# Kernel optimization log

Hardware: AMD Instinct MI355X
Metric: run time of the kernel (lower is better)

Reference implementation:

```python
import jax, jax.numpy as jnp
import numpy as np

C = 32          # d_model / channels
D_STATE = 32
D_CONV = 4
EXPAND = 2
D_INNER = EXPAND * C          # 64
DT_RANK = (C + 15) // 16      # ceil(32/16) = 2
EPS = 1e-5


def _conv2d(x, w, b):
    # x: (B,C,H,W), w: (O,I,3,3), stride 1, padding 1 (torch Conv2d)
    y = jax.lax.conv_general_dilated(
        x, w, window_strides=(1, 1), padding=[(1, 1), (1, 1)],
        dimension_numbers=("NCHW", "OIHW", "NCHW"))
    return y + b[None, :, None, None]


def _silu(x):
    return x * jax.nn.sigmoid(x)


def _mamba(xs, in_proj_w, conv1d_w, conv1d_b, x_proj_w, dt_proj_w, dt_proj_b,
           A_log, Dp, out_proj_w):
    # xs: (B, L, C)
    xz = xs @ in_proj_w.T                       # (B, L, 2*D_INNER)
    xm, z = jnp.split(xz, 2, axis=-1)           # each (B, L, D_INNER)

    # causal depthwise conv1d along L (torch: padding=d_conv-1 then [..., :L])
    xc = xm.transpose(0, 2, 1)                  # (B, D_INNER, L)
    xc = jax.lax.conv_general_dilated(
        xc, conv1d_w, window_strides=(1,), padding=[(D_CONV - 1, 0)],
        dimension_numbers=("NCH", "OIH", "NCH"),
        feature_group_count=D_INNER)
    xm = _silu((xc + conv1d_b[None, :, None]).transpose(0, 2, 1))  # (B,L,D_INNER)

    x_dbl = xm @ x_proj_w.T                     # (B, L, DT_RANK + 2*D_STATE)
    dt = x_dbl[..., :DT_RANK]
    Bm = x_dbl[..., DT_RANK:DT_RANK + D_STATE]  # (B, L, N)
    Cm = x_dbl[..., DT_RANK + D_STATE:]         # (B, L, N)

    delta = jax.nn.softplus(dt @ dt_proj_w.T + dt_proj_b)  # (B, L, D_INNER)
    A = -jnp.exp(A_log)                                     # (D_INNER, N)

    deltaA = jnp.exp(delta[..., None] * A)                           # (B,L,D,N)
    deltaBx = delta[..., None] * Bm[:, :, None, :] * xm[..., None]   # (B,L,D,N)

    def combine(c1, c2):
        a1, b1 = c1
        a2, b2 = c2
        return a1 * a2, a2 * b1 + b2

    # parallel linear recurrence h_t = deltaA_t * h_{t-1} + deltaBx_t
    _, hstate = jax.lax.associative_scan(combine, (deltaA, deltaBx), axis=1)

    y = jnp.einsum("bldn,bln->bld", hstate, Cm) + xm * Dp
    y = y * _silu(z)
    return y @ out_proj_w.T                     # (B, L, C)


def setup_inputs() -> dict:
    key = jax.random.key(0)
    ks = jax.random.split(key, 16)
    s = 0.02
    inp = {
        "x": jax.random.normal(ks[0], (4, C, 64, 64), dtype=jnp.float32),
        "conv1_w": jax.random.normal(ks[1], (2 * C, C, 3, 3), jnp.float32) * s,
        "conv1_b": jnp.zeros((2 * C,), jnp.float32),
        "conv2_w": jax.random.normal(ks[2], (C, 2 * C, 3, 3), jnp.float32) * s,
        "conv2_b": jnp.zeros((C,), jnp.float32),
        "ln_g": jnp.ones((C,), jnp.float32),
        "ln_b": jnp.zeros((C,), jnp.float32),
        "in_proj_w": jax.random.normal(ks[3], (2 * D_INNER, C), jnp.float32) * s,
        "conv1d_w": jax.random.normal(ks[4], (D_INNER, 1, D_CONV), jnp.float32) * 0.1,
        "conv1d_b": jnp.zeros((D_INNER,), jnp.float32),
        "x_proj_w": jax.random.normal(ks[5], (DT_RANK + 2 * D_STATE, D_INNER), jnp.float32) * s,
        "dt_proj_w": jax.random.normal(ks[6], (D_INNER, DT_RANK), jnp.float32) * 0.1,
        "dt_proj_b": jax.random.normal(ks[7], (D_INNER,), jnp.float32) * 0.1 - 4.0,
        "A_log": jnp.log(jnp.tile(jnp.arange(1, D_STATE + 1, dtype=jnp.float32), (D_INNER, 1))),
        "Dp": jnp.ones((D_INNER,), jnp.float32),
        "out_proj_w": jax.random.normal(ks[8], (C, D_INNER), jnp.float32) * s,
        "smooth_w": jax.random.normal(ks[9], (C, C, 3, 3), jnp.float32) * s,
        "smooth_b": jnp.zeros((C,), jnp.float32),
    }
    return inp


def reference(x, conv1_w, conv1_b, conv2_w, conv2_b, ln_g, ln_b,
              in_proj_w, conv1d_w, conv1d_b, x_proj_w, dt_proj_w, dt_proj_b,
              A_log, Dp, out_proj_w, smooth_w, smooth_b):
    b, c, h, w = x.shape
    # convb residual
    t = jax.nn.relu(_conv2d(x, conv1_w, conv1_b))
    x = _conv2d(t, conv2_w, conv2_b) + x
    # reshape (b,c,h,w) -> (b, h*w, c) row-major (faithful to torch .reshape)
    xs = x.reshape(b, -1, c)
    # LayerNorm over last dim
    mu = jnp.mean(xs, axis=-1, keepdims=True)
    var = jnp.mean(jnp.square(xs - mu), axis=-1, keepdims=True)
    xs = (xs - mu) * jax.lax.rsqrt(var + EPS) * ln_g + ln_b
    # Mamba block
    y = _mamba(xs, in_proj_w, conv1d_w, conv1d_b, x_proj_w, dt_proj_w,
               dt_proj_b, A_log, Dp, out_proj_w)
    y = y.transpose(0, 2, 1).reshape(b, c, h, w)
    return _conv2d(y, smooth_w, smooth_b)
```

## Files before the change

kernel.cpp:

```cpp
#include <hip/hip_runtime.h>
#include <math.h>

#define SEQL 4096
#define L2E 1.44269504088896340736f

#if defined(__has_builtin)
#if __has_builtin(__builtin_amdgcn_exp2f)
#define FAST_EXP2(x) __builtin_amdgcn_exp2f(x)
#endif
#endif
#ifndef FAST_EXP2
#define FAST_EXP2(x) exp2f(x)
#endif

__device__ __forceinline__ float sigmoid_f(float x){ return 1.0f/(1.0f+expf(-x)); }

template<int CI, int CO, int COG, bool RELU, bool RES>
__global__ __launch_bounds__(256) void conv3x3_k(const float* __restrict__ in,
    const float* __restrict__ wgt, const float* __restrict__ bias,
    const float* __restrict__ res, float* __restrict__ out)
{
  constexpr int CIT = CI/4;
  __shared__ float tin[4][2][6][72];
  __shared__ float red[3][4][COG][66];
  const int tid  = threadIdx.x;
  const int lane = tid & 63;
  const int ty   = tid >> 6;
  const int tyu  = __builtin_amdgcn_readfirstlane(ty);
  const int h0   = blockIdx.x * 4;
  const int co0  = blockIdx.y * COG;
  const int b    = blockIdx.z;

  if (lane < 24){
    int cl = lane / 12, rem = lane % 12, r = rem >> 1, side = rem & 1;
    tin[ty][cl][r][side ? 68 : 3] = 0.0f;
  }

  float acc[4][COG];
  #pragma unroll
  for (int rr=0;rr<4;++rr)
    #pragma unroll
    for (int u=0;u<COG;++u) acc[rr][u] = 0.0f;

  const int ci0 = tyu*CIT;
  for (int cig = ci0; cig < ci0 + CIT; cig += 2){
    #pragma unroll
    for (int k=0;k<3;++k){
      int idx4 = lane + (k<<6);
      int row  = idx4 >> 4;
      int cl = row/6, r = row - cl*6;
      int w4 = (idx4 & 15) << 2;
      int h  = h0 - 1 + r;
      float4 v = make_float4(0.f,0.f,0.f,0.f);
      if (h>=0 && h<64)
        v = *(const float4*)(in + ((size_t)(b*CI+cig+cl)*64 + h)*64 + w4);
      *(float4*)&tin[ty][cl][r][4+w4] = v;
    }
    #pragma unroll
    for (int cl=0; cl<2; ++cl){
      float rv[6][3];
      #pragma unroll
      for (int r=0;r<6;++r)
        #pragma unroll
        for (int c=0;c<3;++c)
          rv[r][c] = tin[ty][cl][r][3+lane+c];
      #pragma unroll
      for (int u=0;u<COG;++u){
        const float* wp = wgt + ((size_t)(co0+u)*CI + cig + cl)*9;
        #pragma unroll
        for (int rr=0;rr<4;++rr)
          #pragma unroll
          for (int j=0;j<3;++j){
            acc[rr][u] = fmaf(rv[rr+j][0], wp[3*j+0], acc[rr][u]);
            acc[rr][u] = fmaf(rv[rr+j][1], wp[3*j+1], acc[rr][u]);
            acc[rr][u] = fmaf(rv[rr+j][2], wp[3*j+2], acc[rr][u]);
          }
      }
    }
  }
  if (ty > 0){
    #pragma unroll
    for (int rr=0;rr<4;++rr)
      #pragma unroll
      for (int u=0;u<COG;++u) red[ty-1][rr][u][lane] = acc[rr][u];
  }
  __syncthreads();
  if (ty == 0){
    #pragma unroll
    for (int rr=0;rr<4;++rr)
      #pragma unroll
      for (int u=0;u<COG;++u){
        float s = acc[rr][u] + red[0][rr][u][lane] + red[1][rr][u][lane]
                + red[2][rr][u][lane] + bias[co0+u];
        size_t ob = ((size_t)(b*CO+co0+u)*64 + h0+rr)*64 + lane;
        if constexpr (RES)  s += res[ob];
        if constexpr (RELU) s = fmaxf(s, 0.0f);
        out[ob] = s;
      }
  }
}

__global__ __launch_bounds__(1024, 4) void mamba_in_k(const float* __restrict__ x2,
    const float* __restrict__ g, const float* __restrict__ be,
    const float* __restrict__ Wip, const float* __restrict__ cw,
    const float* __restrict__ cb, const float* __restrict__ Wxp,
    const float* __restrict__ Wdt, const float* __restrict__ bdt,
    const float* __restrict__ A_log,
    float* __restrict__ xm2, float* __restrict__ szb, float* __restrict__ dlt,
    float* __restrict__ Bm, float* __restrict__ Cm,
    float* __restrict__ cA, float* __restrict__ cH)
{
  __shared__ __align__(16) float xn[68][37];
  __shared__ __align__(16) float xm[64][68];
  __shared__ __align__(16) float xtT[64][68];
  __shared__ __align__(16) float xd[64][67];
  float (*xbT)[68] = reinterpret_cast<float(*)[68]>(&xn[0][0]);
  const int tid = threadIdx.x, lane = tid & 63, ty = tid >> 6;
  const int tyu = __builtin_amdgcn_readfirstlane(ty);
  const int bi = blockIdx.x >> 6;
  const int l0 = (blockIdx.x & 63) << 6;

  {
    const int row = tid >> 3, sub = tid & 7;
    if (row < 67){
      const int tok = l0 - 3 + row;
      const int c0 = sub << 2;
      if (tok >= 0){
        float4 f = *(const float4*)(x2 + (size_t)bi*131072 + (size_t)tok*32 + c0);
        float s = (f.x+f.y)+(f.z+f.w);
        s += __shfl_xor(s,1); s += __shfl_xor(s,2); s += __shfl_xor(s,4);
        const float mu = s * 0.03125f;
        float dx=f.x-mu, dy=f.y-mu, dz=f.z-mu, dw=f.w-mu;
        float q = (dx*dx+dy*dy)+(dz*dz+dw*dw);
        q += __shfl_xor(q,1); q += __shfl_xor(q,2); q += __shfl_xor(q,4);
        const float rstd = 1.0f/sqrtf(q*0.03125f + 1e-5f);
        float4 gv = *(const float4*)(g  + c0);
        float4 bv = *(const float4*)(be + c0);
        xn[row][c0+0] = dx*rstd*gv.x + bv.x;
        xn[row][c0+1] = dy*rstd*gv.y + bv.y;
        xn[row][c0+2] = dz*rstd*gv.z + bv.z;
        xn[row][c0+3] = dw*rstd*gv.w + bv.w;
      } else {
        xn[row][c0+0]=0.0f; xn[row][c0+1]=0.0f;
        xn[row][c0+2]=0.0f; xn[row][c0+3]=0.0f;
      }
    }
  }
  __syncthreads();

  if (ty < 8){
    const int d0 = tyu*8;
    float xvA[32];
    #pragma unroll
    for (int c=0;c<32;++c) xvA[c] = xn[lane][c];
    #pragma unroll
    for (int jj=0;jj<8;++jj){
      const float4* wr = (const float4*)(Wip + (d0+jj)*32);
      float a = 0.0f;
      #pragma unroll
      for (int c4=0;c4<8;++c4){
        float4 w = wr[c4];
        a = fmaf(xvA[c4*4+0], w.x, a);
        a = fmaf(xvA[c4*4+1], w.y, a);
        a = fmaf(xvA[c4*4+2], w.z, a);
        a = fmaf(xvA[c4*4+3], w.w, a);
      }
      xm[d0+jj][lane] = a;
    }
    if (lane < 3){
      float xvB[32];
      #pragma unroll
      for (int c=0;c<32;++c) xvB[c] = xn[64+lane][c];
      #pragma unroll
      for (int jj=0;jj<8;++jj){
        const float4* wr = (const float4*)(Wip + (d0+jj)*32);
        float a = 0.0f;
        #pragma unroll
        for (int c4=0;c4<8;++c4){
          float4 w = wr[c4];
          a = fmaf(xvB[c4*4+0], w.x, a);
          a = fmaf(xvB[c4*4+1], w.y, a);
          a = fmaf(xvB[c4*4+2], w.z, a);
          a = fmaf(xvB[c4*4+3], w.w, a);
        }
        xm[d0+jj][64+lane] = a;
      }
    }
  } else {
    const int d0z = (tyu-8)*8;
    float xvC[32];
    #pragma unroll
    for (int c=0;c<32;++c) xvC[c] = xn[lane+3][c];
    #pragma unroll
    for (int jj=0;jj<8;++jj){
      const float4* wr = (const float4*)(Wip + (64+d0z+jj)*32);
      float a = 0.0f;
      #pragma unroll
      for (int c4=0;c4<8;++c4){
        float4 w = wr[c4];
        a = fmaf(xvC[c4*4+0], w.x, a);
        a = fmaf(xvC[c4*4+1], w.y, a);
        a = fmaf(xvC[c4*4+2], w.z, a);
        a = fmaf(xvC[c4*4+3], w.w, a);
      }
      szb[((size_t)(bi*64+d0z+jj))*SEQL + l0 + lane] = a * sigmoid_f(a);
    }
  }
  __syncthreads();

  #pragma unroll
  for (int jj=0;jj<4;++jj){
    int d = tyu*4 + jj;
    float4 w = *(const float4*)(cw + d*4);
    float a = xm[d][lane]*w.x + xm[d][lane+1]*w.y
            + xm[d][lane+2]*w.z + xm[d][lane+3]*w.w + cb[d];
    float s = a * sigmoid_f(a);
    xtT[d][lane] = s;
    xm2[((size_t)(bi*64+d))*SEQL + l0 + lane] = s;
  }
  __syncthreads();

  {
    float xv[64];
    #pragma unroll
    for (int c=0;c<64;++c) xv[c] = xtT[c][lane];
    for (int j=tyu; j<66; j+=16){
      const float4* wr = (const float4*)(Wxp + j*64);
      float a = 0.0f;
      #pragma unroll
      for (int c4=0;c4<16;++c4){
        float4 w = wr[c4];
        a = fmaf(xv[c4*4+0], w.x, a);
        a = fmaf(xv[c4*4+1], w.y, a);
        a = fmaf(xv[c4*4+2], w.z, a);
        a = fmaf(xv[c4*4+3], w.w, a);
      }
      xd[lane][j] = a;
    }
  }
  __syncthreads();

  {
    float dt0 = xd[lane][0], dt1 = xd[lane][1];
    #pragma unroll
    for (int k=0;k<4;++k){
      int d2 = tyu*4 + k;
      float2 wd = *(const float2*)(Wdt + d2*2);
      float v = dt0*wd.x + dt1*wd.y + bdt[d2];
      float sp = fmaxf(v,0.0f) + log1pf(expf(-fabsf(v)));
      dlt[((size_t)(bi*64+d2))*SEQL + l0 + lane] = sp;
      xm[d2][lane] = sp;
    }
    const int which = tyu >> 3, gq = tyu & 7;
    float* dst = which ? Cm : Bm;
    size_t base = ((size_t)bi*SEQL + l0 + lane)*32 + gq*4;
    const int s2 = 2 + which*32;
    float4 f0;
    f0.x = xd[lane][s2+gq+ 0]; f0.y = xd[lane][s2+gq+ 8];
    f0.z = xd[lane][s2+gq+16]; f0.w = xd[lane][s2+gq+24];
    *(float4*)(dst + base) = f0;
    if (!which){
      xbT[gq     ][lane] = f0.x;
      xbT[gq +  8][lane] = f0.y;
      xbT[gq + 16][lane] = f0.z;
      xbT[gq + 24][lane] = f0.w;
    }
  }
  __syncthreads();

  {
    const int d  = tid >> 4;
    const int gg = tid & 15;
    const int chunk = blockIdx.x & 63;
    const int bd = bi*64 + d;
    float Av0 = -expf(A_log[d*32 + gg     ]) * L2E;
    float Av1 = -expf(A_log[d*32 + gg + 16]) * L2E;
    float h0=0.0f, h1=0.0f, aP0=1.0f, aP1=1.0f;
    #pragma unroll 2
    for (int t0=0;t0<64;t0+=4){
      float4 dl4 = *(const float4*)&xm [d    ][t0];
      float4 xs4 = *(const float4*)&xtT[d    ][t0];
      float4 b04 = *(const float4*)&xbT[gg   ][t0];
      float4 b14 = *(const float4*)&xbT[gg+16][t0];
      #pragma unroll
      for (int k=0;k<4;++k){
        float dlv = (k==0)? dl4.x : (k==1)? dl4.y : (k==2)? dl4.z : dl4.w;
        float xsv = (k==0)? xs4.x : (k==1)? xs4.y : (k==2)? xs4.z : xs4.w;
        float bv0 = (k==0)? b04.x : (k==1)? b04.y : (k==2)? b04.z : b04.w;
        float bv1 = (k==0)? b14.x : (k==1)? b14.y : (k==2)? b14.z : b14.w;
        float m  = dlv * xsv;
        float a0 = FAST_EXP2(dlv*Av0);
        float a1 = FAST_EXP2(dlv*Av1);
        h0 = fmaf(a0, h0, m*bv0);  aP0 *= a0;
        h1 = fmaf(a1, h1, m*bv1);  aP1 *= a1;
      }
    }
    size_t base = ((size_t)bd*64 + chunk)*32;
    cA[base + gg] = aP0; cA[base + gg + 16] = aP1;
    cH[base + gg] = h0;  cH[base + gg + 16] = h1;
  }
}

__global__ __launch_bounds__(256) void scan_p2(const float* __restrict__ dlt,
    const float* __restrict__ xssm, const float* __restrict__ Bm,
    const float* __restrict__ Cm, const float* __restrict__ A_log,
    const float* __restrict__ Dp, const float* __restrict__ sz,
    const float* __restrict__ cA, const float* __restrict__ cHs,
    float* __restrict__ yt)
{
  __shared__ float pre[32][34];
  const int tid = threadIdx.x;
  const int grp = blockIdx.x & 1;
  const int bd  = blockIdx.x >> 1;
  const int b = bd >> 6, d = bd & 63;
  const int c0 = grp << 5;

  if (tid < 32){
    const float* pa = cA  + (size_t)bd*2048 + tid;
    const float* ph = cHs + (size_t)bd*2048 + tid;
    float hrun = 0.0f;
    if (grp){
      #pragma unroll 4
      for (int c=0;c<32;++c)
        hrun = fmaf(pa[c*32], hrun, ph[c*32]);
    }
    #pragma unroll 4
    for (int k=0;k<32;++k){
      pre[tid][k] = hrun;
      hrun = fmaf(pa[(c0+k)*32], hrun, ph[(c0+k)*32]);
    }
  }
  __syncthreads();

  const int lc = tid >> 3, gg = tid & 7;
  const int chunk = c0 + lc;
  const int l0 = chunk << 6;
  const float Dv = Dp[d];
  float Av2[4], h[4];
  #pragma unroll
  for (int j=0;j<4;++j){
    Av2[j] = -expf(A_log[d*32 + gg + 8*j]) * L2E;
    h[j] = pre[gg + 8*j][lc];
  }
  const float* del = dlt  + (size_t)bd*SEQL + l0;
  const float* xp  = xssm + (size_t)bd*SEQL + l0;
  const float* szp = sz   + (size_t)bd*SEQL + l0;
  const float* Bp  = Bm + ((size_t)b*SEQL + l0)*32 + gg*4;
  const float* Cp  = Cm + ((size_t)b*SEQL + l0)*32 + gg*4;
  float* yp = yt + (size_t)bd*SEQL + l0;

  for (int i0=0;i0<64;i0+=16){
    float4 y4[4];
    #pragma unroll
    for (int s=0;s<4;++s){
      const int ib = i0 + s*4;
      float4 d4 = *(const float4*)(del+ib);
      float4 x4 = *(const float4*)(xp +ib);
      float4 s4 = *(const float4*)(szp+ib);
      #pragma unroll
      for (int t=0;t<4;++t){
        float dl = (t==0)? d4.x : (t==1)? d4.y : (t==2)? d4.z : d4.w;
        float xl = (t==0)? x4.x : (t==1)? x4.y : (t==2)? x4.z : x4.w;
        float sl = (t==0)? s4.x : (t==1)? s4.y : (t==2)? s4.z : s4.w;
        float4 bv = *(const float4*)(Bp + (ib+t)*32);
        float4 cv = *(const float4*)(Cp + (ib+t)*32);
        float a0 = FAST_EXP2(dl*Av2[0]); h[0] = fmaf(a0, h[0], dl*bv.x*xl);
        float a1 = FAST_EXP2(dl*Av2[1]); h[1] = fmaf(a1, h[1], dl*bv.y*xl);
        float a2 = FAST_EXP2(dl*Av2[2]); h[2] = fmaf(a2, h[2], dl*bv.z*xl);
        float a3 = FAST_EXP2(dl*Av2[3]); h[3] = fmaf(a3, h[3], dl*bv.w*xl);
        float v = fmaf(h[3], cv.w, fmaf(h[2], cv.z, fmaf(h[1], cv.y, h[0]*cv.x)));
        v += __shfl_xor(v,1); v += __shfl_xor(v,2); v += __shfl_xor(v,4);
        float yv = fmaf(xl, Dv, v) * sl;
        if      (t==0) y4[s].x = yv;
        else if (t==1) y4[s].y = yv;
        else if (t==2) y4[s].z = yv;
        else           y4[s].w = yv;
      }
    }
    if (gg < 4){
      float4 w = (gg==0) ? y4[0] : (gg==1) ? y4[1] : (gg==2) ? y4[2] : y4[3];
      *(float4*)(yp + i0 + gg*4) = w;
    }
  }
}

__global__ __launch_bounds__(512) void outproj_k(const float* __restrict__ yt,
    const float* __restrict__ Wout, float* __restrict__ ym)
{
  __shared__ float ys[64][67];
  const int tid = threadIdx.x, lane = tid & 63, ty = tid >> 6;
  const int tyu = __builtin_amdgcn_readfirstlane(ty);
  const int bi = blockIdx.x >> 6;
  const int l0 = (blockIdx.x & 63) << 6;
  for (int r=ty; r<64; r+=8)
    ys[lane][r] = yt[((size_t)(bi*64+r))*SEQL + l0 + lane];
  __syncthreads();
  float yv[64];
  #pragma unroll
  for (int c=0;c<64;++c) yv[c] = ys[lane][c];
  #pragma unroll
  for (int jj=0;jj<4;++jj){
    int j = tyu*4 + jj;
    const float4* wr = (const float4*)(Wout + j*64);
    float acc = 0.0f;
    #pragma unroll
    for (int c4=0;c4<16;++c4){
      float4 w = wr[c4];
      acc = fmaf(yv[c4*4+0], w.x, acc);
      acc = fmaf(yv[c4*4+1], w.y, acc);
      acc = fmaf(yv[c4*4+2], w.z, acc);
      acc = fmaf(yv[c4*4+3], w.w, acc);
    }
    ym[((size_t)(bi*32+j))*SEQL + l0 + lane] = acc;
  }
}

extern "C" void kernel_launch(void* const* d_in, const int* in_sizes, int n_in,
                              void* d_out, int out_size, void* d_ws, size_t ws_size,
                              hipStream_t stream) {
  const float* x        = (const float*)d_in[0];
  const float* conv1_w  = (const float*)d_in[1];
  const float* conv1_b  = (const float*)d_in[2];
  const float* conv2_w  = (const float*)d_in[3];
  const float* conv2_b  = (const float*)d_in[4];
  const float* ln_g     = (const float*)d_in[5];
  const float* ln_b     = (const float*)d_in[6];
  const float* in_proj_w= (const float*)d_in[7];
  const float* conv1d_w = (const float*)d_in[8];
  const float* conv1d_b = (const float*)d_in[9];
  const float* x_proj_w = (const float*)d_in[10];
  const float* dt_proj_w= (const float*)d_in[11];
  const float* dt_proj_b= (const float*)d_in[12];
  const float* A_log    = (const float*)d_in[13];
  const float* Dp       = (const float*)d_in[14];
  const float* out_proj_w=(const float*)d_in[15];
  const float* smooth_w = (const float*)d_in[16];
  const float* smooth_b = (const float*)d_in[17];
  float* out = (float*)d_out;

  float* ws = (float*)d_ws;
  float* t      = ws;
  float* x2     = t      + 1048576;
  float* xm2    = x2     + 524288;
  float* szb    = xm2    + 1048576;
  float* dlt    = szb    + 1048576;
  float* Bmat   = dlt    + 1048576;
  float* Cmat   = Bmat   + 524288;
  float* yt     = Cmat   + 524288;
  float* ym     = yt     + 1048576;
  float* cA     = t;
  float* cH     = t + 524288;

  conv3x3_k<32,64,4,true ,false><<<dim3(16,16,4), 256, 0, stream>>>(x,  conv1_w, conv1_b, nullptr, t);
  conv3x3_k<64,32,4,false,true ><<<dim3(16,8,4), 256, 0, stream>>>(t,  conv2_w, conv2_b, x,       x2);
  mamba_in_k  <<<256, 1024, 0, stream>>>(x2, ln_g, ln_b, in_proj_w, conv1d_w, conv1d_b,
                                         x_proj_w, dt_proj_w, dt_proj_b, A_log,
                                         xm2, szb, dlt, Bmat, Cmat, cA, cH);
  scan_p2     <<<512, 256, 0, stream>>>(dlt, xm2, Bmat, Cmat, A_log, Dp, szb, cA, cH, yt);
  outproj_k   <<<256, 512, 0, stream>>>(yt, out_proj_w, ym);
  conv3x3_k<32,32,4,false,false><<<dim3(16,8,4), 256, 0, stream>>>(ym, smooth_w, smooth_b, nullptr, out);
}
```

Baseline: 192.1 us.

## Fuse chunked scan second pass with output projection in one kernel

Replaces the separate scan pass-2 and out-projection kernels with a single kernel. Each block handles one batch and one 64-token chunk for all 64 channels, stages delta, x, z, B and C through shared memory, computes each thread's chunk-prefix state by serially combining earlier chunk summaries, and applies the out projection directly from shared memory. This removes the intermediate y buffer round trip through global memory and one kernel launch. The cost is a per-thread serial prefix loop of up to 63 steps over chunk summaries, which adds redundant global reads and latency for later chunks.

```diff
diff --git a/kernel.cpp b/kernel.cpp
--- a/kernel.cpp
+++ b/kernel.cpp
@@ -301,117 +301,110 @@
   }
 }
 
-__global__ __launch_bounds__(256) void scan_p2(const float* __restrict__ dlt,
-    const float* __restrict__ xssm, const float* __restrict__ Bm,
-    const float* __restrict__ Cm, const float* __restrict__ A_log,
-    const float* __restrict__ Dp, const float* __restrict__ sz,
+__global__ __launch_bounds__(1024, 4) void mamba_out_k(const float* __restrict__ dlt,
+    const float* __restrict__ xssm, const float* __restrict__ szb,
+    const float* __restrict__ Bm, const float* __restrict__ Cm,
+    const float* __restrict__ A_log, const float* __restrict__ Dp,
     const float* __restrict__ cA, const float* __restrict__ cHs,
-    float* __restrict__ yt)
-{
-  __shared__ float pre[32][34];
-  const int tid = threadIdx.x;
-  const int grp = blockIdx.x & 1;
-  const int bd  = blockIdx.x >> 1;
-  const int b = bd >> 6, d = bd & 63;
-  const int c0 = grp << 5;
-
-  if (tid < 32){
-    const float* pa = cA  + (size_t)bd*2048 + tid;
-    const float* ph = cHs + (size_t)bd*2048 + tid;
-    float hrun = 0.0f;
-    if (grp){
-      #pragma unroll 4
-      for (int c=0;c<32;++c)
-        hrun = fmaf(pa[c*32], hrun, ph[c*32]);
-    }
-    #pragma unroll 4
-    for (int k=0;k<32;++k){
-      pre[tid][k] = hrun;
-      hrun = fmaf(pa[(c0+k)*32], hrun, ph[(c0+k)*32]);
-    }
-  }
-  __syncthreads();
-
-  const int lc = tid >> 3, gg = tid & 7;
-  const int chunk = c0 + lc;
-  const int l0 = chunk << 6;
-  const float Dv = Dp[d];
-  float Av2[4], h[4];
-  #pragma unroll
-  for (int j=0;j<4;++j){
-    Av2[j] = -expf(A_log[d*32 + gg + 8*j]) * L2E;
-    h[j] = pre[gg + 8*j][lc];
-  }
-  const float* del = dlt  + (size_t)bd*SEQL + l0;
-  const float* xp  = xssm + (size_t)bd*SEQL + l0;
-  const float* szp = sz   + (size_t)bd*SEQL + l0;
-  const float* Bp  = Bm + ((size_t)b*SEQL + l0)*32 + gg*4;
-  const float* Cp  = Cm + ((size_t)b*SEQL + l0)*32 + gg*4;
-  float* yp = yt + (size_t)bd*SEQL + l0;
-
-  for (int i0=0;i0<64;i0+=16){
-    float4 y4[4];
-    #pragma unroll
-    for (int s=0;s<4;++s){
-      const int ib = i0 + s*4;
-      float4 d4 = *(const float4*)(del+ib);
-      float4 x4 = *(const float4*)(xp +ib);
-      float4 s4 = *(const float4*)(szp+ib);
-      #pragma unroll
-      for (int t=0;t<4;++t){
-        float dl = (t==0)? d4.x : (t==1)? d4.y : (t==2)? d4.z : d4.w;
-        float xl = (t==0)? x4.x : (t==1)? x4.y : (t==2)? x4.z : x4.w;
-        float sl = (t==0)? s4.x : (t==1)? s4.y : (t==2)? s4.z : s4.w;
-        float4 bv = *(const float4*)(Bp + (ib+t)*32);
-        float4 cv = *(const float4*)(Cp + (ib+t)*32);
-        float a0 = FAST_EXP2(dl*Av2[0]); h[0] = fmaf(a0, h[0], dl*bv.x*xl);
-        float a1 = FAST_EXP2(dl*Av2[1]); h[1] = fmaf(a1, h[1], dl*bv.y*xl);
-        float a2 = FAST_EXP2(dl*Av2[2]); h[2] = fmaf(a2, h[2], dl*bv.z*xl);
-        float a3 = FAST_EXP2(dl*Av2[3]); h[3] = fmaf(a3, h[3], dl*bv.w*xl);
-        float v = fmaf(h[3], cv.w, fmaf(h[2], cv.z, fmaf(h[1], cv.y, h[0]*cv.x)));
-        v += __shfl_xor(v,1); v += __shfl_xor(v,2); v += __shfl_xor(v,4);
-        float yv = fmaf(xl, Dv, v) * sl;
-        if      (t==0) y4[s].x = yv;
-        else if (t==1) y4[s].y = yv;
-        else if (t==2) y4[s].z = yv;
-        else           y4[s].w = yv;
-      }
-    }
-    if (gg < 4){
-      float4 w = (gg==0) ? y4[0] : (gg==1) ? y4[1] : (gg==2) ? y4[2] : y4[3];
-      *(float4*)(yp + i0 + gg*4) = w;
-    }
-  }
-}
-
-__global__ __launch_bounds__(512) void outproj_k(const float* __restrict__ yt,
     const float* __restrict__ Wout, float* __restrict__ ym)
 {
-  __shared__ float ys[64][67];
+  __shared__ __align__(16) float dl32[64][36];
+  __shared__ __align__(16) float xs32[64][36];
+  __shared__ __align__(16) float z32 [64][36];
+  __shared__ __align__(16) float B32 [32][36];
+  __shared__ __align__(16) float ct32[32][34];
+  __shared__ __align__(16) float ysT [64][68];
   const int tid = threadIdx.x, lane = tid & 63, ty = tid >> 6;
   const int tyu = __builtin_amdgcn_readfirstlane(ty);
   const int bi = blockIdx.x >> 6;
-  const int l0 = (blockIdx.x & 63) << 6;
-  for (int r=ty; r<64; r+=8)
-    ys[lane][r] = yt[((size_t)(bi*64+r))*SEQL + l0 + lane];
-  __syncthreads();
-  float yv[64];
+  const int chunk = blockIdx.x & 63;
+  const int l0 = chunk << 6;
+
+  const int d = tid >> 4, gg = tid & 15;
+  const int bd = bi*64 + d;
+  const float Av0 = -expf(A_log[d*32 + gg     ]) * L2E;
+  const float Av1 = -expf(A_log[d*32 + gg + 16]) * L2E;
+  const float Dv  = Dp[d];
+
+  float h0 = 0.0f, h1 = 0.0f;
+  {
+    const float* pa = cA  + (size_t)bd*64*32;
+    const float* ph = cHs + (size_t)bd*64*32;
+    #pragma unroll 4
+    for (int c = 0; c < chunk; ++c){
+      float a0 = pa[c*32 + gg     ], q0 = ph[c*32 + gg     ];
+      float a1 = pa[c*32 + gg + 16], q1 = ph[c*32 + gg + 16];
+      h0 = fmaf(a0, h0, q0);
+      h1 = fmaf(a1, h1, q1);
+    }
+  }
+
   #pragma unroll
-  for (int c=0;c<64;++c) yv[c] = ys[lane][c];
-  #pragma unroll
-  for (int jj=0;jj<4;++jj){
-    int j = tyu*4 + jj;
-    const float4* wr = (const float4*)(Wout + j*64);
-    float acc = 0.0f;
-    #pragma unroll
-    for (int c4=0;c4<16;++c4){
-      float4 w = wr[c4];
-      acc = fmaf(yv[c4*4+0], w.x, acc);
-      acc = fmaf(yv[c4*4+1], w.y, acc);
-      acc = fmaf(yv[c4*4+2], w.z, acc);
-      acc = fmaf(yv[c4*4+3], w.w, acc);
-    }
-    ym[((size_t)(bi*32+j))*SEQL + l0 + lane] = acc;
+  for (int s = 0; s < 2; ++s){
+    const int t0 = s << 5;
+    if (tid < 512){
+      int dd = tid >> 3, f = (tid & 7) << 2;
+      *(float4*)&dl32[dd][f] = *(const float4*)(dlt + (size_t)(bi*64+dd)*SEQL + l0 + t0 + f);
+      *(float4*)&z32 [dd][f] = *(const float4*)(szb + (size_t)(bi*64+dd)*SEQL + l0 + t0 + f);
+    } else {
+      int u = tid - 512;
+      int dd = u >> 3, f = (u & 7) << 2;
+      *(float4*)&xs32[dd][f] = *(const float4*)(xssm + (size_t)(bi*64+dd)*SEQL + l0 + t0 + f);
+      if (u < 256){
+        int tok = u >> 3, q = u & 7;
+        float4 fb = *(const float4*)(Bm + ((size_t)(bi*SEQL) + l0 + t0 + tok)*32 + q*4);
+        B32[q     ][tok] = fb.x;
+        B32[q +  8][tok] = fb.y;
+        B32[q + 16][tok] = fb.z;
+        B32[q + 24][tok] = fb.w;
+      } else {
+        int v = u - 256;
+        int tok = v >> 3, q = v & 7;
+        float4 fc = *(const float4*)(Cm + ((size_t)(bi*SEQL) + l0 + t0 + tok)*32 + q*4);
+        ct32[tok][q     ] = fc.x;
+        ct32[tok][q +  8] = fc.y;
+        ct32[tok][q + 16] = fc.z;
+        ct32[tok][q + 24] = fc.w;
+      }
+    }
+    __syncthreads();
+
+    #pragma unroll 4
+    for (int t = 0; t < 32; ++t){
+      float dlv = dl32[d][t];
+      float xsv = xs32[d][t];
+      float m   = dlv * xsv;
+      float bv0 = B32[gg   ][t];
+      float bv1 = B32[gg+16][t];
+      float a0 = FAST_EXP2(dlv*Av0);
+      float a1 = FAST_EXP2(dlv*Av1);
+      h0 = fmaf(a0, h0, m*bv0);
+      h1 = fmaf(a1, h1, m*bv1);
+      float part = fmaf(h1, ct32[t][gg+16], h0*ct32[t][gg]);
+      part += __shfl_xor(part,1); part += __shfl_xor(part,2);
+      part += __shfl_xor(part,4); part += __shfl_xor(part,8);
+      if (gg == 0)
+        ysT[d][t0 + t] = fmaf(xsv, Dv, part) * z32[d][t];
+    }
+    __syncthreads();
+  }
+
+  {
+    const float4* w0 = (const float4*)(Wout + tyu*64);
+    const float4* w1 = (const float4*)(Wout + (tyu+16)*64);
+    float a0 = 0.0f, a1 = 0.0f;
+    #pragma unroll
+    for (int c4 = 0; c4 < 16; ++c4){
+      float4 wa = w0[c4], wb = w1[c4];
+      float y0 = ysT[c4*4+0][lane];
+      float y1 = ysT[c4*4+1][lane];
+      float y2 = ysT[c4*4+2][lane];
+      float y3 = ysT[c4*4+3][lane];
+      a0 = fmaf(y3, wa.w, fmaf(y2, wa.z, fmaf(y1, wa.y, fmaf(y0, wa.x, a0))));
+      a1 = fmaf(y3, wb.w, fmaf(y2, wb.z, fmaf(y1, wb.y, fmaf(y0, wb.x, a1))));
+    }
+    ym[(size_t)(bi*32 + tyu     )*SEQL + l0 + lane] = a0;
+    ym[(size_t)(bi*32 + tyu + 16)*SEQL + l0 + lane] = a1;
   }
 }
 
@@ -446,8 +439,7 @@
   float* dlt    = szb    + 1048576;
   float* Bmat   = dlt    + 1048576;
   float* Cmat   = Bmat   + 524288;
-  float* yt     = Cmat   + 524288;
-  float* ym     = yt     + 1048576;
+  float* ym     = Cmat   + 524288;
   float* cA     = t;
   float* cH     = t + 524288;
 
@@ -456,7 +448,7 @@
   mamba_in_k  <<<256, 1024, 0, stream>>>(x2, ln_g, ln_b, in_proj_w, conv1d_w, conv1d_b,
                                          x_proj_w, dt_proj_w, dt_proj_b, A_log,
                                          xm2, szb, dlt, Bmat, Cmat, cA, cH);
-  scan_p2     <<<512, 256, 0, stream>>>(dlt, xm2, Bmat, Cmat, A_log, Dp, szb, cA, cH, yt);
-  outproj_k   <<<256, 512, 0, stream>>>(yt, out_proj_w, ym);
+  mamba_out_k <<<256, 1024, 0, stream>>>(dlt, xm2, szb, Bmat, Cmat, A_log, Dp,
+                                         cA, cH, out_proj_w, ym);
   conv3x3_k<32,32,4,false,false><<<dim3(16,8,4), 256, 0, stream>>>(ym, smooth_w, smooth_b, nullptr, out);
 }
```

Result: no change. 193.4 us (+0.6%).

## Restructure 3x3 conv to split output channels across waves, drop LDS reduction

Applied to the files above, without the earlier changes.

The conv3x3 kernel no longer splits input channels across the four waves with a shared-memory partial-sum reduction. Each wave now owns its own group of output channels over all input channels, with a 32-channel input tile staged cooperatively in LDS. Each block covers 2 output rows instead of 4, and the launch grids change to 32x2x4 blocks. The goal is to remove the reduction barrier and idle waves in the epilogue and to reuse each staged input tile across more output channels. The cost is fewer blocks (256) and more serialized work per wave over the input channels.

```diff
diff --git a/kernel.cpp b/kernel.cpp
--- a/kernel.cpp
+++ b/kernel.cpp
@@ -15,88 +15,82 @@
 
 __device__ __forceinline__ float sigmoid_f(float x){ return 1.0f/(1.0f+expf(-x)); }
 
-template<int CI, int CO, int COG, bool RELU, bool RES>
+template<int CI, int CO, int COW, bool RELU, bool RES>
 __global__ __launch_bounds__(256) void conv3x3_k(const float* __restrict__ in,
     const float* __restrict__ wgt, const float* __restrict__ bias,
     const float* __restrict__ res, float* __restrict__ out)
 {
-  constexpr int CIT = CI/4;
-  __shared__ float tin[4][2][6][72];
-  __shared__ float red[3][4][COG][66];
+  constexpr int NST = CI / 32;
+  __shared__ __align__(16) float tin[32][4][72];
   const int tid  = threadIdx.x;
   const int lane = tid & 63;
   const int ty   = tid >> 6;
   const int tyu  = __builtin_amdgcn_readfirstlane(ty);
-  const int h0   = blockIdx.x * 4;
-  const int co0  = blockIdx.y * COG;
+  const int h0   = blockIdx.x * 2;
+  const int co0  = blockIdx.y * (4*COW) + tyu*COW;
   const int b    = blockIdx.z;
 
-  if (lane < 24){
-    int cl = lane / 12, rem = lane % 12, r = rem >> 1, side = rem & 1;
-    tin[ty][cl][r][side ? 68 : 3] = 0.0f;
-  }
-
-  float acc[4][COG];
-  #pragma unroll
-  for (int rr=0;rr<4;++rr)
-    #pragma unroll
-    for (int u=0;u<COG;++u) acc[rr][u] = 0.0f;
-
-  const int ci0 = tyu*CIT;
-  for (int cig = ci0; cig < ci0 + CIT; cig += 2){
-    #pragma unroll
-    for (int k=0;k<3;++k){
-      int idx4 = lane + (k<<6);
-      int row  = idx4 >> 4;
-      int cl = row/6, r = row - cl*6;
-      int w4 = (idx4 & 15) << 2;
-      int h  = h0 - 1 + r;
+  float acc[2][COW];
+  #pragma unroll
+  for (int rr=0;rr<2;++rr)
+    #pragma unroll
+    for (int u=0;u<COW;++u) acc[rr][u] = 0.0f;
+
+  for (int st=0; st<NST; ++st){
+    const int cig = st*32;
+    if (st) __syncthreads();
+    #pragma unroll
+    for (int k=0;k<8;++k){
+      int i   = tid + (k<<8);
+      int ci  = i >> 6;
+      int rem = i & 63;
+      int row = rem >> 4;
+      int w4  = (rem & 15) << 2;
+      int h   = h0 - 1 + row;
       float4 v = make_float4(0.f,0.f,0.f,0.f);
       if (h>=0 && h<64)
-        v = *(const float4*)(in + ((size_t)(b*CI+cig+cl)*64 + h)*64 + w4);
-      *(float4*)&tin[ty][cl][r][4+w4] = v;
-    }
-    #pragma unroll
-    for (int cl=0; cl<2; ++cl){
-      float rv[6][3];
-      #pragma unroll
-      for (int r=0;r<6;++r)
+        v = *(const float4*)(in + ((size_t)(b*CI+cig+ci)*64 + h)*64 + w4);
+      *(float4*)&tin[ci][row][4+w4] = v;
+      if (w4 == 0)  tin[ci][row][3]  = 0.0f;
+      if (w4 == 60) tin[ci][row][68] = 0.0f;
+    }
+    __syncthreads();
+    #pragma unroll 4
+    for (int ci=0; ci<32; ++ci){
+      float rv[4][3];
+      #pragma unroll
+      for (int r=0;r<4;++r)
         #pragma unroll
         for (int c=0;c<3;++c)
-          rv[r][c] = tin[ty][cl][r][3+lane+c];
-      #pragma unroll
-      for (int u=0;u<COG;++u){
-        const float* wp = wgt + ((size_t)(co0+u)*CI + cig + cl)*9;
+          rv[r][c] = tin[ci][r][3+lane+c];
+      #pragma unroll
+      for (int u=0;u<COW;++u){
+        const float* wp = wgt + ((size_t)(co0+u)*CI + cig + ci)*9;
         #pragma unroll
-        for (int rr=0;rr<4;++rr)
+        for (int j=0;j<3;++j){
+          float w0 = wp[3*j+0], w1 = wp[3*j+1], w2 = wp[3*j+2];
           #pragma unroll
-          for (int j=0;j<3;++j){
-            acc[rr][u] = fmaf(rv[rr+j][0], wp[3*j+0], acc[rr][u]);
-            acc[rr][u] = fmaf(rv[rr+j][1], wp[3*j+1], acc[rr][u]);
-            acc[rr][u] = fmaf(rv[rr+j][2], wp[3*j+2], acc[rr][u]);
+          for (int rr=0;rr<2;++rr){
+            acc[rr][u] = fmaf(rv[rr+j][0], w0, acc[rr][u]);
+            acc[rr][u] = fmaf(rv[rr+j][1], w1, acc[rr][u]);
+            acc[rr][u] = fmaf(rv[rr+j][2], w2, acc[rr][u]);
           }
-      }
-    }
-  }
-  if (ty > 0){
-    #pragma unroll
-    for (int rr=0;rr<4;++rr)
-      #pragma unroll
-      for (int u=0;u<COG;++u) red[ty-1][rr][u][lane] = acc[rr][u];
-  }
-  __syncthreads();
-  if (ty == 0){
-    #pragma unroll
-    for (int rr=0;rr<4;++rr)
-      #pragma unroll
-      for (int u=0;u<COG;++u){
-        float s = acc[rr][u] + red[0][rr][u][lane] + red[1][rr][u][lane]
-                + red[2][rr][u][lane] + bias[co0+u];
-        size_t ob = ((size_t)(b*CO+co0+u)*64 + h0+rr)*64 + lane;
-        if constexpr (RES)  s += res[ob];
-        if constexpr (RELU) s = fmaxf(s, 0.0f);
-        out[ob] = s;
-      }
+        }
+      }
+    }
+  }
+
+  #pragma unroll
+  for (int u=0;u<COW;++u){
+    const float bv = bias[co0+u];
+    #pragma unroll
+    for (int rr=0;rr<2;++rr){
+      float s = acc[rr][u] + bv;
+      size_t ob = ((size_t)(b*CO+co0+u)*64 + h0+rr)*64 + lane;
+      if constexpr (RES)  s += res[ob];
+      if constexpr (RELU) s = fmaxf(s, 0.0f);
+      out[ob] = s;
+    }
   }
 }
 
@@ -451,12 +445,12 @@
   float* cA     = t;
   float* cH     = t + 524288;
 
-  conv3x3_k<32,64,4,true ,false><<<dim3(16,16,4), 256, 0, stream>>>(x,  conv1_w, conv1_b, nullptr, t);
-  conv3x3_k<64,32,4,false,true ><<<dim3(16,8,4), 256, 0, stream>>>(t,  conv2_w, conv2_b, x,       x2);
+  conv3x3_k<32,64,8,true ,false><<<dim3(32,2,4), 256, 0, stream>>>(x,  conv1_w, conv1_b, nullptr, t);
+  conv3x3_k<64,32,4,false,true ><<<dim3(32,2,4), 256, 0, stream>>>(t,  conv2_w, conv2_b, x,       x2);
   mamba_in_k  <<<256, 1024, 0, stream>>>(x2, ln_g, ln_b, in_proj_w, conv1d_w, conv1d_b,
                                          x_proj_w, dt_proj_w, dt_proj_b, A_log,
                                          xm2, szb, dlt, Bmat, Cmat, cA, cH);
   scan_p2     <<<512, 256, 0, stream>>>(dlt, xm2, Bmat, Cmat, A_log, Dp, szb, cA, cH, yt);
   outproj_k   <<<256, 512, 0, stream>>>(yt, out_proj_w, ym);
-  conv3x3_k<32,32,4,false,false><<<dim3(16,8,4), 256, 0, stream>>>(ym, smooth_w, smooth_b, nullptr, out);
+  conv3x3_k<32,32,4,false,false><<<dim3(32,2,4), 256, 0, stream>>>(ym, smooth_w, smooth_b, nullptr, out);
 }
```

Result: slower. 232.4 us (+21.0%).
